# Optimization experiments

Measured on AMD Instinct MI355X. Metric: run time of the kernel, lower is better.

Reference implementation:

```python
import jax, jax.numpy as jnp
import numpy as np

DIM = 768
NUM_HEADS = 12
HEAD_DIM = DIM // NUM_HEADS
TIME_STEPS = 4
TAU_MEM = 2.0
THRESH = 1.0
NOISE_PROB = 0.01


def setup_inputs() -> dict:
    key = jax.random.key(0)
    ks = jax.random.split(key, 9)
    B, N = 8, 1024
    s = 1.0 / np.sqrt(DIM)
    inp = {"x": jax.random.normal(ks[0], (B, N, DIM), jnp.float32)}
    for i, nm in enumerate(["q", "k", "v", "o"]):
        inp["W" + nm] = jax.random.normal(ks[1 + i], (DIM, DIM), jnp.float32) * s
        inp["b" + nm] = jax.random.normal(ks[5 + i], (DIM,), jnp.float32) * 0.01
    return inp


def _lif_spikes(inp):
    """Multi-step LIF: constant input each step, leaky integrate, hard threshold,
    soft reset; aggregated spikes clamped to 1 (binary). Straight-through sigmoid
    surrogate keeps the op differentiable without changing forward values."""
    decay = jnp.exp(jnp.asarray(-1.0 / TAU_MEM, inp.dtype))

    def step(v, _):
        v = v * decay + inp
        sur = jax.nn.sigmoid(4.0 * (v - THRESH))
        hard = (v >= THRESH).astype(inp.dtype)
        spike = jax.lax.stop_gradient(hard - sur) + sur
        v = v - THRESH * spike
        return v, spike

    _, spikes = jax.lax.scan(step, jnp.zeros_like(inp), None, length=TIME_STEPS)
    # sum over time then clamp(max=1.0) -> binary aggregate spike map
    return jnp.minimum(spikes.sum(axis=0), 1.0)


def reference(x, Wq, bq, Wk, bk, Wv, bv, Wo, bo):
    B, N, C = x.shape
    q_lin = x @ Wq.T + bq
    k_lin = x @ Wk.T + bk
    v_lin = x @ Wv.T + bv

    s_q = _lif_spikes(q_lin)  # (B,N,C) binary
    s_k = _lif_spikes(k_lin)
    s_v = _lif_spikes(v_lin)

    # noise injection for fully-silent samples (deterministic key)
    silent = jnp.all(s_q == 0, axis=(1, 2)) & jnp.all(s_k == 0, axis=(1, 2))  # (B,)
    nk = jax.random.split(jax.random.key(42), 2)
    noise_q = (jax.random.uniform(nk[0], s_q.shape) < NOISE_PROB).astype(s_q.dtype)
    noise_k = (jax.random.uniform(nk[1], s_k.shape) < NOISE_PROB).astype(s_k.dtype)
    s_q = jnp.where(silent[:, None, None], jnp.maximum(s_q, noise_q), s_q)
    s_k = jnp.where(silent[:, None, None], jnp.maximum(s_k, noise_k), s_k)

    # (B,H,N,Dh)
    s_q = s_q.reshape(B, N, NUM_HEADS, HEAD_DIM).transpose(0, 2, 1, 3)
    s_k = s_k.reshape(B, N, NUM_HEADS, HEAD_DIM).transpose(0, 2, 1, 3)
    s_v = s_v.reshape(B, N, NUM_HEADS, HEAD_DIM).transpose(0, 2, 1, 3)

    # XNOR similarity: sum_d (1 - (q-k)^2) = Dh - |q| - |k| + 2 q.k  (exact, since
    # the broadcast form expands to the same polynomial; q,k binary so q^2=q)
    q2 = jnp.sum(s_q * s_q, axis=-1)  # (B,H,N)
    k2 = jnp.sum(s_k * s_k, axis=-1)  # (B,H,N)
    qk = jnp.einsum('bhnd,bhmd->bhnm', s_q, s_k)
    scores = HEAD_DIM - q2[..., :, None] - k2[..., None, :] + 2.0 * qk  # (B,H,N,N)

    attn = jax.nn.sigmoid(scores)
    out = jnp.einsum('bhnm,bhmd->bhnd', attn, s_v)  # (B,H,N,Dh)
    out = out.transpose(0, 2, 1, 3).reshape(B, N, C)
    return out @ Wo.T + bo
```

## Files before the change

kernel.cpp:

```cpp
#include <hip/hip_runtime.h>


typedef __attribute__((ext_vector_type(8))) short short8;
typedef __attribute__((ext_vector_type(4))) float f32x4;
typedef __attribute__((ext_vector_type(2))) unsigned long long u64x2;
typedef unsigned long long u64;

static __device__ __forceinline__ unsigned short f2bf(float f) {
  unsigned int u = __builtin_bit_cast(unsigned int, f);
  return (unsigned short)((u + 0x7FFFu + ((u >> 16) & 1u)) >> 16);
}

static __device__ __forceinline__ u64 pack4bf(float a, float b, float c, float d) {
  return (u64)f2bf(a) | ((u64)f2bf(b) << 16) | ((u64)f2bf(c) << 32) |
         ((u64)f2bf(d) << 48);
}

static __device__ __forceinline__ void gl2lds16(const unsigned short* g,
                                                unsigned short* l) {
  __builtin_amdgcn_global_load_lds(
      (const __attribute__((address_space(1))) unsigned int*)(g),
      (__attribute__((address_space(3))) unsigned int*)(l),
      16, 0, 0);
}

__global__ void k_convert(const float* __restrict__ x,
                          const float* __restrict__ Wq, const float* __restrict__ bq,
                          const float* __restrict__ Wk, const float* __restrict__ bk,
                          const float* __restrict__ Wv, const float* __restrict__ bv,
                          unsigned short* __restrict__ xb,
                          unsigned short* __restrict__ wcat,
                          float* __restrict__ bcat,
                          int* __restrict__ cnt,
                          float* __restrict__ colsum) {
  const int X4 = 1572864;
  const int W4 = 147456;
  const int NB = 576;
  const int NZ = 1536;
  const int total = X4 + 3 * W4 + NB + NZ;
  int t = blockIdx.x * blockDim.x + threadIdx.x;
  if (t >= total) return;
  if (t == 0) *cnt = 0;
  if (t < X4) {
    float4 v = ((const float4*)x)[t];
    *(u64*)(xb + 4 * (long)t) = pack4bf(v.x, v.y, v.z, v.w);
  } else if (t < X4 + 3 * W4) {
    int j = t - X4;
    const float* src = Wq;
    int jj = j;
    if (jj >= 2 * W4) { src = Wv; jj -= 2 * W4; }
    else if (jj >= W4) { src = Wk; jj -= W4; }
    float4 v = ((const float4*)src)[jj];
    *(u64*)(wcat + 4 * (long)j) = pack4bf(v.x, v.y, v.z, v.w);
  } else if (t < X4 + 3 * W4 + NB) {
    int j = t - (X4 + 3 * W4);
    int idx = j * 4;
    const float* src = bq;
    int ii = idx;
    if (ii >= 1536) { src = bv; ii -= 1536; }
    else if (ii >= 768) { src = bk; ii -= 768; }
    float4 v = *(const float4*)(src + ii);
    *(float4*)(bcat + idx) = v;
  } else {
    int j = t - (X4 + 3 * W4 + NB);
    float4 z = {0.f, 0.f, 0.f, 0.f};
    ((float4*)colsum)[j] = z;
  }
}

__global__ __launch_bounds__(256, 4)
void k_qkv(const unsigned short* __restrict__ xb,
           const unsigned short* __restrict__ wcat,
           const float* __restrict__ bcat,
           u64* __restrict__ bits3,
           float* __restrict__ colsum)
{
  __shared__ __align__(16) unsigned short lA[128 * 64];
  __shared__ __align__(16) unsigned short lB[128 * 64];
  const int tid = threadIdx.x;
  const int lane = tid & 63;
  const int wid = tid >> 6;
  const int wm = wid >> 1, wn = wid & 1;
  const int row0 = blockIdx.x * 128;
  const int col0 = blockIdx.y * 128;
  const int srow = lane >> 3;
  const int scol = (lane & 7) * 8;
  const int rr = lane & 15;
  const int g = lane >> 4;
  const int g8 = g * 8;

  const unsigned short* gA = xb + (long)(row0 + wid * 32 + srow) * 768 + scol;
  const unsigned short* gB = wcat + (long)(col0 + wid * 32 + srow) * 768 + scol;
  unsigned short* sA = &lA[(wid * 32 + srow) * 64 + scol];
  unsigned short* sB = &lB[(wid * 32 + srow) * 64 + scol];

  f32x4 acc[4][4] = {};

#pragma unroll 1
  for (int kt = 0; kt < 768; kt += 64) {
    __syncthreads();
#pragma unroll
    for (int s = 0; s < 4; ++s) {
      gl2lds16(gA + s * (8 * 768) + kt, sA + s * (8 * 64));
      gl2lds16(gB + s * (8 * 768) + kt, sB + s * (8 * 64));
    }
    __syncthreads();
#pragma unroll
    for (int kk = 0; kk < 2; ++kk) {
      const int ko = kk * 32 + g8;
      short8 af[4];
#pragma unroll
      for (int i = 0; i < 4; ++i)
        af[i] = *(const short8*)&lA[(wm * 64 + i * 16 + rr) * 64 + ko];
#pragma unroll
      for (int j = 0; j < 4; ++j) {
        const short8 bf = *(const short8*)&lB[(wn * 64 + j * 16 + rr) * 64 + ko];
#pragma unroll
        for (int i = 0; i < 4; ++i)
          acc[i][j] = __builtin_amdgcn_mfma_f32_16x16x32_bf16(af[i], bf, acc[i][j], 0, 0, 0);
      }
    }
  }

  const int mi = blockIdx.y / 6;
  const int h = 2 * (blockIdx.y - mi * 6) + wn;
  u64* bits = bits3 + (long)mi * 98304;
  const float C_LIF = 0.45505041f;
  float thr[4];
#pragma unroll
  for (int j = 0; j < 4; ++j) thr[j] = C_LIF - bcat[col0 + wn * 64 + j * 16 + rr];

  float csum[4] = {0.f, 0.f, 0.f, 0.f};
#pragma unroll
  for (int i = 0; i < 4; ++i) {
#pragma unroll
    for (int r = 0; r < 4; ++r) {
      u64 map = 0;
#pragma unroll
      for (int j = 0; j < 4; ++j) {
        const bool sp = acc[i][j][r] >= thr[j];
        const u64 bl = __ballot(sp);
        map |= ((bl >> (g * 16)) & 0xFFFFull) << (j * 16);
        csum[j] += sp ? 1.0f : 0.0f;
      }
      if (rr == 0) {
        const int grow = row0 + wm * 64 + i * 16 + g * 4 + r;
        const int b = grow >> 10, n = grow & 1023;
        bits[((long)b * 12 + h) * 1024 + n] = map;
      }
    }
  }
  if (mi == 2) {
    const int b = row0 >> 10;
#pragma unroll
    for (int j = 0; j < 4; ++j) {
      float s = csum[j];
      s += __shfl_xor(s, 16);
      s += __shfl_xor(s, 32);
      if (lane < 16) atomicAdd(colsum + b * 768 + h * 64 + j * 16 + rr, s);
    }
  }
}

__global__ __launch_bounds__(256)
void k_sb(const u64* __restrict__ qbits, const u64* __restrict__ kbits,
          const float* __restrict__ colsum, const float* __restrict__ Wo,
          const float* __restrict__ bo,
          int* __restrict__ cnt, int4* __restrict__ list,
          float* __restrict__ base) {
  __shared__ __align__(16) u64 kb[1024];
  const int tid = threadIdx.x;
  const int bid = blockIdx.x;
  if (bid < 768) {
    const int bh = bid >> 3;
    const u64* src = kbits + (long)bh * 1024;
#pragma unroll
    for (int u = 0; u < 4; ++u) kb[tid * 4 + u] = src[tid * 4 + u];
    __syncthreads();
    const int n = (bid & 7) * 128 + (tid >> 1);
    const u64 qb = qbits[(long)bh * 1024 + n];
    const u64x2* kb2 = (const u64x2*)kb + (tid & 1) * 256;
    int mh = 0;
#pragma unroll 4
    for (int mm = 0; mm < 256; ++mm) {
      const u64x2 v = kb2[mm];
      mh = max(mh, __popcll(qb ^ v.x));
      mh = max(mh, __popcll(qb ^ v.y));
    }
    const int rowmax = max(mh, __shfl_xor(mh, 1));
    if (rowmax > 52) {
      const int mbase = (tid & 1) * 512;
      for (int mm = 0; mm < 512; ++mm) {
        const int hd = __popcll(qb ^ kb[mbase + mm]);
        if (hd > 52) {
          const int e = atomicAdd(cnt, 1);
          if (e < 8192) list[e] = make_int4(bh, n, mbase + mm, hd);
        }
      }
    }
  } else {
    const int bb = bid - 768;
    const int b = bb / 3, ch = bb - b * 3;
    const int oc = ch * 256 + tid;
    const float4* c4 = (const float4*)(colsum + b * 768);
    const float4* w4 = (const float4*)(Wo + (long)oc * 768);
    float acc = bo[oc];
#pragma unroll 4
    for (int i = 0; i < 192; ++i) {
      const float4 c = c4[i], w = w4[i];
      acc += c.x * w.x + c.y * w.y + c.z * w.z + c.w * w.w;
    }
    base[b * 768 + oc] = acc;
  }
}

__global__ __launch_bounds__(192)
void k_out(const float* __restrict__ base, const int* __restrict__ cnt,
           const int4* __restrict__ list, const u64* __restrict__ vbits,
           const float* __restrict__ Wo, float* __restrict__ out) {
  const int row = blockIdx.x;
  const int b = row >> 10;
  float4 v = ((const float4*)(base + b * 768))[threadIdx.x];
  const int c = min(*cnt, 8192);
  if (c > 0) {
    const int n = row & 1023;
    for (int e = 0; e < c; ++e) {
      const int4 E = list[e];
      const int eb = E.x / 12;
      if (eb == b && E.y == n) {
        const int hh = E.x - eb * 12;
        const float s = (float)(64 - E.w);
        const float w = 1.0f / (1.0f + __expf(s));
        const u64 vb = vbits[(long)E.x * 1024 + E.z];
        float4 d = {0.f, 0.f, 0.f, 0.f};
        for (int dd = 0; dd < 64; ++dd)
          if ((vb >> dd) & 1ull) {
            const float* wp = Wo + (long)(threadIdx.x * 4) * 768 + hh * 64 + dd;
            d.x += wp[0]; d.y += wp[768]; d.z += wp[1536]; d.w += wp[2304];
          }
        v.x -= w * d.x; v.y -= w * d.y; v.z -= w * d.z; v.w -= w * d.w;
      }
    }
  }
  ((float4*)(out + (long)row * 768))[threadIdx.x] = v;
}

extern "C" void kernel_launch(void* const* d_in, const int* in_sizes, int n_in,
                              void* d_out, int out_size, void* d_ws, size_t ws_size,
                              hipStream_t stream) {
  const float* x  = (const float*)d_in[0];
  const float* Wq = (const float*)d_in[1];
  const float* bq = (const float*)d_in[2];
  const float* Wk = (const float*)d_in[3];
  const float* bk = (const float*)d_in[4];
  const float* Wv = (const float*)d_in[5];
  const float* bv = (const float*)d_in[6];
  const float* Wo = (const float*)d_in[7];
  const float* bo = (const float*)d_in[8];
  float* out = (float*)d_out;

  char* ws = (char*)d_ws;
  unsigned short* xb    = (unsigned short*)(ws + 0);
  unsigned short* wcat  = (unsigned short*)(ws + 12582912);
  float*          bcat  = (float*)(ws + 16121856);
  u64*            bits3 = (u64*)(ws + 16131072);
  float*          colsum = (float*)(ws + 18490368);
  float*          base   = (float*)(ws + 18514944);
  int*            cnt    = (int*)(ws + 18539520);
  int4*           list   = (int4*)(ws + 18539536);

  const u64* qbits = bits3;
  const u64* kbits = bits3 + 98304;
  const u64* vbits = bits3 + 2 * 98304;

  k_convert<<<dim3(7881), dim3(256), 0, stream>>>(x, Wq, bq, Wk, bk, Wv, bv,
                                                  xb, wcat, bcat, cnt, colsum);
  k_qkv<<<dim3(64, 18), dim3(256), 0, stream>>>(xb, wcat, bcat, bits3, colsum);
  k_sb<<<dim3(792), dim3(256), 0, stream>>>(qbits, kbits, colsum, Wo, bo,
                                            cnt, list, base);
  k_out<<<dim3(8192), dim3(192), 0, stream>>>(base, cnt, list, vbits, Wo, out);
}
```

Measured before the change: 101.6 us.

## Prune Hamming-distance candidate scan by bucketing keys by popcount

Keys for each head are counting-sorted in shared memory by popcount, using a histogram and suffix sums. Each query row then scans only the keys whose popcount is large enough that popcount(q^k) could exceed the threshold, since popcount(q^k) <= popcount(q)+popcount(k). This replaces the full 1024-key max pass plus rescan with a bounded candidate scan. The cost is extra shared memory, LDS atomics, and a serial prefix-sum loop on one thread.

```diff
diff --git a/kernel.cpp b/kernel.cpp
--- a/kernel.cpp
+++ b/kernel.cpp
@@ -3,7 +3,6 @@
 
 typedef __attribute__((ext_vector_type(8))) short short8;
 typedef __attribute__((ext_vector_type(4))) float f32x4;
-typedef __attribute__((ext_vector_type(2))) unsigned long long u64x2;
 typedef unsigned long long u64;
 
 static __device__ __forceinline__ unsigned short f2bf(float f) {
@@ -169,33 +168,55 @@
           int* __restrict__ cnt, int4* __restrict__ list,
           float* __restrict__ base) {
   __shared__ __align__(16) u64 kb[1024];
+  __shared__ int pkv[1024];
+  __shared__ unsigned short cand[1024];
+  __shared__ int hist[65];
+  __shared__ int sufv[65];
   const int tid = threadIdx.x;
   const int bid = blockIdx.x;
   if (bid < 768) {
     const int bh = bid >> 3;
     const u64* src = kbits + (long)bh * 1024;
-#pragma unroll
-    for (int u = 0; u < 4; ++u) kb[tid * 4 + u] = src[tid * 4 + u];
+    if (tid < 65) hist[tid] = 0;
+    __syncthreads();
+#pragma unroll
+    for (int u = 0; u < 4; ++u) {
+      const int m = tid + 256 * u;
+      const u64 v = src[m];
+      kb[m] = v;
+      const int pk = __popcll(v);
+      pkv[m] = pk;
+      atomicAdd(&hist[pk], 1);
+    }
+    __syncthreads();
+    if (tid == 0) {
+      int run = 0;
+#pragma unroll 1
+      for (int v = 64; v >= 0; --v) {
+        const int c = hist[v];
+        hist[v] = run;
+        run += c;
+        sufv[v] = run;
+      }
+    }
+    __syncthreads();
+#pragma unroll
+    for (int u = 0; u < 4; ++u) {
+      const int m = tid + 256 * u;
+      const int pos = atomicAdd(&hist[pkv[m]], 1);
+      cand[pos] = (unsigned short)m;
+    }
     __syncthreads();
     const int n = (bid & 7) * 128 + (tid >> 1);
     const u64 qb = qbits[(long)bh * 1024 + n];
-    const u64x2* kb2 = (const u64x2*)kb + (tid & 1) * 256;
-    int mh = 0;
-#pragma unroll 4
-    for (int mm = 0; mm < 256; ++mm) {
-      const u64x2 v = kb2[mm];
-      mh = max(mh, __popcll(qb ^ v.x));
-      mh = max(mh, __popcll(qb ^ v.y));
-    }
-    const int rowmax = max(mh, __shfl_xor(mh, 1));
-    if (rowmax > 52) {
-      const int mbase = (tid & 1) * 512;
-      for (int mm = 0; mm < 512; ++mm) {
-        const int hd = __popcll(qb ^ kb[mbase + mm]);
-        if (hd > 52) {
-          const int e = atomicAdd(cnt, 1);
-          if (e < 8192) list[e] = make_int4(bh, n, mbase + mm, hd);
-        }
+    const int t = 53 - __popcll(qb);
+    const int L = (t <= 0) ? 1024 : ((t > 64) ? 0 : sufv[t]);
+    for (int e = (tid & 1); e < L; e += 2) {
+      const int m = cand[e];
+      const int hd = __popcll(qb ^ kb[m]);
+      if (hd > 52) {
+        const int x = atomicAdd(cnt, 1);
+        if (x < 8192) list[x] = make_int4(bh, n, m, hd);
       }
     }
   } else {
```

New measurement: 117.9 us. 16.1% more time.

## Prefilter high-popcount q/k rows in QKV kernel to prune Hamming search

Applied to the files above, without the earlier changes.

The QKV kernel now records, per (batch, head), the row indices whose q or k spike word has popcount of at least 27 into small candidate lists. The Hamming-distance search kernel then only compares those candidate q rows against all k rows, and the remaining low-popcount q rows against only the candidate k rows. This replaces the all-pairs 1024x1024 popcount scan per head. The colsum·Wo base computation is also remapped onto fewer blocks. The result is exact only if a pair can exceed the distance threshold of 52 only when one side has popcount of at least 27, and only if no list overflows its 128-entry cap. Overflow would silently drop pairs.

```diff
diff --git a/kernel.cpp b/kernel.cpp
--- a/kernel.cpp
+++ b/kernel.cpp
@@ -3,7 +3,6 @@
 
 typedef __attribute__((ext_vector_type(8))) short short8;
 typedef __attribute__((ext_vector_type(4))) float f32x4;
-typedef __attribute__((ext_vector_type(2))) unsigned long long u64x2;
 typedef unsigned long long u64;
 
 static __device__ __forceinline__ unsigned short f2bf(float f) {
@@ -32,11 +31,12 @@
                           unsigned short* __restrict__ wcat,
                           float* __restrict__ bcat,
                           int* __restrict__ cnt,
-                          float* __restrict__ colsum) {
+                          float* __restrict__ colsum,
+                          int* __restrict__ hiCnt) {
   const int X4 = 1572864;
   const int W4 = 147456;
   const int NB = 576;
-  const int NZ = 1536;
+  const int NZ = 1584;
   const int total = X4 + 3 * W4 + NB + NZ;
   int t = blockIdx.x * blockDim.x + threadIdx.x;
   if (t >= total) return;
@@ -64,7 +64,8 @@
   } else {
     int j = t - (X4 + 3 * W4 + NB);
     float4 z = {0.f, 0.f, 0.f, 0.f};
-    ((float4*)colsum)[j] = z;
+    if (j < 1536) ((float4*)colsum)[j] = z;
+    else          ((float4*)hiCnt)[j - 1536] = z;
   }
 }
 
@@ -73,7 +74,9 @@
            const unsigned short* __restrict__ wcat,
            const float* __restrict__ bcat,
            u64* __restrict__ bits3,
-           float* __restrict__ colsum)
+           float* __restrict__ colsum,
+           int* __restrict__ hiCnt,
+           unsigned short* __restrict__ hiList)
 {
   __shared__ __align__(16) unsigned short lA[128 * 64];
   __shared__ __align__(16) unsigned short lB[128 * 64];
@@ -146,7 +149,14 @@
       if (rr == 0) {
         const int grow = row0 + wm * 64 + i * 16 + g * 4 + r;
         const int b = grow >> 10, n = grow & 1023;
-        bits[((long)b * 12 + h) * 1024 + n] = map;
+        const int bh = b * 12 + h;
+        bits[(long)bh * 1024 + n] = map;
+        if (mi < 2) {
+          if (__popcll(map) >= 27) {
+            const int p = atomicAdd(hiCnt + mi * 96 + bh, 1);
+            if (p < 128) hiList[(mi * 96 + bh) * 128 + p] = (unsigned short)n;
+          }
+        }
       }
     }
   }
@@ -164,44 +174,53 @@
 
 __global__ __launch_bounds__(256)
 void k_sb(const u64* __restrict__ qbits, const u64* __restrict__ kbits,
+          const int* __restrict__ hiCnt, const unsigned short* __restrict__ hiList,
           const float* __restrict__ colsum, const float* __restrict__ Wo,
           const float* __restrict__ bo,
           int* __restrict__ cnt, int4* __restrict__ list,
           float* __restrict__ base) {
-  __shared__ __align__(16) u64 kb[1024];
   const int tid = threadIdx.x;
-  const int bid = blockIdx.x;
-  if (bid < 768) {
-    const int bh = bid >> 3;
-    const u64* src = kbits + (long)bh * 1024;
-#pragma unroll
-    for (int u = 0; u < 4; ++u) kb[tid * 4 + u] = src[tid * 4 + u];
+  const int bh = blockIdx.x;
+  const int y = blockIdx.y;
+  if (y < 128) {
+    const int nc = min(hiCnt[bh], 128);
+    if (y >= nc) return;
+    const int n = hiList[bh * 128 + y];
+    const u64 qv = qbits[(long)bh * 1024 + n];
+    const u64* kp = kbits + (long)bh * 1024;
+#pragma unroll
+    for (int u = 0; u < 4; ++u) {
+      const int m = tid + 256 * u;
+      const int hd = __popcll(qv ^ kp[m]);
+      if (hd > 52) {
+        const int x = atomicAdd(cnt, 1);
+        if (x < 8192) list[x] = make_int4(bh, n, m, hd);
+      }
+    }
+  } else if (y < 136) {
+    __shared__ u64 kd[128];
+    __shared__ unsigned short km[128];
+    const int kc = min(hiCnt[96 + bh], 128);
+    if (tid < kc) {
+      const int m = hiList[(96 + bh) * 128 + tid];
+      km[tid] = (unsigned short)m;
+      kd[tid] = kbits[(long)bh * 1024 + m];
+    }
     __syncthreads();
-    const int n = (bid & 7) * 128 + (tid >> 1);
-    const u64 qb = qbits[(long)bh * 1024 + n];
-    const u64x2* kb2 = (const u64x2*)kb + (tid & 1) * 256;
-    int mh = 0;
-#pragma unroll 4
-    for (int mm = 0; mm < 256; ++mm) {
-      const u64x2 v = kb2[mm];
-      mh = max(mh, __popcll(qb ^ v.x));
-      mh = max(mh, __popcll(qb ^ v.y));
-    }
-    const int rowmax = max(mh, __shfl_xor(mh, 1));
-    if (rowmax > 52) {
-      const int mbase = (tid & 1) * 512;
-      for (int mm = 0; mm < 512; ++mm) {
-        const int hd = __popcll(qb ^ kb[mbase + mm]);
-        if (hd > 52) {
-          const int e = atomicAdd(cnt, 1);
-          if (e < 8192) list[e] = make_int4(bh, n, mbase + mm, hd);
-        }
+    const int n = (y - 128) * 128 + (tid >> 1);
+    const u64 qv = qbits[(long)bh * 1024 + n];
+    if (__popcll(qv) >= 27) return;
+    for (int e = (tid & 1); e < kc; e += 2) {
+      const int hd = __popcll(qv ^ kd[e]);
+      if (hd > 52) {
+        const int x = atomicAdd(cnt, 1);
+        if (x < 8192) list[x] = make_int4(bh, n, km[e], hd);
       }
     }
   } else {
-    const int bb = bid - 768;
-    const int b = bb / 3, ch = bb - b * 3;
-    const int oc = ch * 256 + tid;
+    if (bh >= 24) return;
+    const int oc = bh * 32 + (tid >> 3);
+    const int b = tid & 7;
     const float4* c4 = (const float4*)(colsum + b * 768);
     const float4* w4 = (const float4*)(Wo + (long)oc * 768);
     float acc = bo[oc];
@@ -260,23 +279,27 @@
   float* out = (float*)d_out;
 
   char* ws = (char*)d_ws;
-  unsigned short* xb    = (unsigned short*)(ws + 0);
-  unsigned short* wcat  = (unsigned short*)(ws + 12582912);
-  float*          bcat  = (float*)(ws + 16121856);
-  u64*            bits3 = (u64*)(ws + 16131072);
+  unsigned short* xb     = (unsigned short*)(ws + 0);
+  unsigned short* wcat   = (unsigned short*)(ws + 12582912);
+  float*          bcat   = (float*)(ws + 16121856);
+  u64*            bits3  = (u64*)(ws + 16131072);
   float*          colsum = (float*)(ws + 18490368);
   float*          base   = (float*)(ws + 18514944);
   int*            cnt    = (int*)(ws + 18539520);
   int4*           list   = (int4*)(ws + 18539536);
+  int*            hiCnt  = (int*)(ws + 18670608);
+  unsigned short* hiList = (unsigned short*)(ws + 18671376);
 
   const u64* qbits = bits3;
   const u64* kbits = bits3 + 98304;
   const u64* vbits = bits3 + 2 * 98304;
 
   k_convert<<<dim3(7881), dim3(256), 0, stream>>>(x, Wq, bq, Wk, bk, Wv, bv,
-                                                  xb, wcat, bcat, cnt, colsum);
-  k_qkv<<<dim3(64, 18), dim3(256), 0, stream>>>(xb, wcat, bcat, bits3, colsum);
-  k_sb<<<dim3(792), dim3(256), 0, stream>>>(qbits, kbits, colsum, Wo, bo,
-                                            cnt, list, base);
+                                                  xb, wcat, bcat, cnt, colsum,
+                                                  hiCnt);
+  k_qkv<<<dim3(64, 18), dim3(256), 0, stream>>>(xb, wcat, bcat, bits3, colsum,
+                                                hiCnt, hiList);
+  k_sb<<<dim3(96, 137), dim3(256), 0, stream>>>(qbits, kbits, hiCnt, hiList,
+                                                colsum, Wo, bo, cnt, list, base);
   k_out<<<dim3(8192), dim3(192), 0, stream>>>(base, cnt, list, vbits, Wo, out);
 }
```

Result: slower. 117.4 us (+15.5%).

## Prune Hamming search with popcount-filtered key lists and per-row correction in output kernel

Applied to the files above, without the earlier changes.

Replaces the brute-force all-pairs Hamming scan over every (query,key) pair with a pigeonhole filter. Any pair with Hamming distance above 52 needs both popcounts large or small, so keys with popcount of at least 27 are compacted into per-head lists. Each output row then scans the full key set only when its query has a high popcount, and otherwise only the compacted list, collecting hits in shared memory. This drops the global atomic list and the per-row scan of that list in the output kernel, and changes the base GEMV mapping to cover all batches per block. It risks truncating hits at 64 per row.

```diff
diff --git a/kernel.cpp b/kernel.cpp
--- a/kernel.cpp
+++ b/kernel.cpp
@@ -3,7 +3,6 @@
 
 typedef __attribute__((ext_vector_type(8))) short short8;
 typedef __attribute__((ext_vector_type(4))) float f32x4;
-typedef __attribute__((ext_vector_type(2))) unsigned long long u64x2;
 typedef unsigned long long u64;
 
 static __device__ __forceinline__ unsigned short f2bf(float f) {
@@ -31,7 +30,6 @@
                           unsigned short* __restrict__ xb,
                           unsigned short* __restrict__ wcat,
                           float* __restrict__ bcat,
-                          int* __restrict__ cnt,
                           float* __restrict__ colsum) {
   const int X4 = 1572864;
   const int W4 = 147456;
@@ -40,7 +38,6 @@
   const int total = X4 + 3 * W4 + NB + NZ;
   int t = blockIdx.x * blockDim.x + threadIdx.x;
   if (t >= total) return;
-  if (t == 0) *cnt = 0;
   if (t < X4) {
     float4 v = ((const float4*)x)[t];
     *(u64*)(xb + 4 * (long)t) = pack4bf(v.x, v.y, v.z, v.w);
@@ -163,45 +160,38 @@
 }
 
 __global__ __launch_bounds__(256)
-void k_sb(const u64* __restrict__ qbits, const u64* __restrict__ kbits,
-          const float* __restrict__ colsum, const float* __restrict__ Wo,
-          const float* __restrict__ bo,
-          int* __restrict__ cnt, int4* __restrict__ list,
-          float* __restrict__ base) {
-  __shared__ __align__(16) u64 kb[1024];
+void k_hg(const u64* __restrict__ kbits, const float* __restrict__ colsum,
+          const float* __restrict__ Wo, const float* __restrict__ bo,
+          int* __restrict__ hiCnt, unsigned short* __restrict__ hiIdx,
+          u64* __restrict__ hiData, float* __restrict__ base) {
   const int tid = threadIdx.x;
   const int bid = blockIdx.x;
-  if (bid < 768) {
-    const int bh = bid >> 3;
-    const u64* src = kbits + (long)bh * 1024;
-#pragma unroll
-    for (int u = 0; u < 4; ++u) kb[tid * 4 + u] = src[tid * 4 + u];
-    __syncthreads();
-    const int n = (bid & 7) * 128 + (tid >> 1);
-    const u64 qb = qbits[(long)bh * 1024 + n];
-    const u64x2* kb2 = (const u64x2*)kb + (tid & 1) * 256;
-    int mh = 0;
-#pragma unroll 4
-    for (int mm = 0; mm < 256; ++mm) {
-      const u64x2 v = kb2[mm];
-      mh = max(mh, __popcll(qb ^ v.x));
-      mh = max(mh, __popcll(qb ^ v.y));
-    }
-    const int rowmax = max(mh, __shfl_xor(mh, 1));
-    if (rowmax > 52) {
-      const int mbase = (tid & 1) * 512;
-      for (int mm = 0; mm < 512; ++mm) {
-        const int hd = __popcll(qb ^ kb[mbase + mm]);
-        if (hd > 52) {
-          const int e = atomicAdd(cnt, 1);
-          if (e < 8192) list[e] = make_int4(bh, n, mbase + mm, hd);
-        }
-      }
+  if (bid < 96) {
+    __shared__ int cnt_l;
+    __shared__ unsigned short lst[1024];
+    if (tid == 0) cnt_l = 0;
+    __syncthreads();
+    const u64* src = kbits + (long)bid * 1024;
+#pragma unroll
+    for (int u = 0; u < 4; ++u) {
+      const int m = tid + u * 256;
+      if (__popcll(src[m]) >= 27) {
+        const int p = atomicAdd(&cnt_l, 1);
+        lst[p] = (unsigned short)m;
+      }
+    }
+    __syncthreads();
+    const int c = cnt_l;
+    if (tid == 0) hiCnt[bid] = c;
+    for (int p = tid; p < c; p += 256) {
+      const int m = lst[p];
+      hiIdx[bid * 1024 + p] = (unsigned short)m;
+      hiData[(long)bid * 1024 + p] = src[m];
     }
   } else {
-    const int bb = bid - 768;
-    const int b = bb / 3, ch = bb - b * 3;
-    const int oc = ch * 256 + tid;
+    const int j = bid - 96;
+    const int oc = j * 32 + (tid >> 3);
+    const int b = tid & 7;
     const float4* c4 = (const float4*)(colsum + b * 768);
     const float4* w4 = (const float4*)(Wo + (long)oc * 768);
     float acc = bo[oc];
@@ -215,34 +205,57 @@
 }
 
 __global__ __launch_bounds__(192)
-void k_out(const float* __restrict__ base, const int* __restrict__ cnt,
-           const int4* __restrict__ list, const u64* __restrict__ vbits,
-           const float* __restrict__ Wo, float* __restrict__ out) {
+void k_out(const float* __restrict__ base, const u64* __restrict__ qbits,
+           const u64* __restrict__ kbits, const int* __restrict__ hiCnt,
+           const unsigned short* __restrict__ hiIdx, const u64* __restrict__ hiData,
+           const u64* __restrict__ vbits, const float* __restrict__ Wo,
+           float* __restrict__ out) {
+  __shared__ int vc;
+  __shared__ int vm[64], vh[64], vhd[64];
+  const int tid = threadIdx.x;
   const int row = blockIdx.x;
-  const int b = row >> 10;
-  float4 v = ((const float4*)(base + b * 768))[threadIdx.x];
-  const int c = min(*cnt, 8192);
-  if (c > 0) {
-    const int n = row & 1023;
-    for (int e = 0; e < c; ++e) {
-      const int4 E = list[e];
-      const int eb = E.x / 12;
-      if (eb == b && E.y == n) {
-        const int hh = E.x - eb * 12;
-        const float s = (float)(64 - E.w);
-        const float w = 1.0f / (1.0f + __expf(s));
-        const u64 vb = vbits[(long)E.x * 1024 + E.z];
-        float4 d = {0.f, 0.f, 0.f, 0.f};
-        for (int dd = 0; dd < 64; ++dd)
-          if ((vb >> dd) & 1ull) {
-            const float* wp = Wo + (long)(threadIdx.x * 4) * 768 + hh * 64 + dd;
-            d.x += wp[0]; d.y += wp[768]; d.z += wp[1536]; d.w += wp[2304];
-          }
-        v.x -= w * d.x; v.y -= w * d.y; v.z -= w * d.z; v.w -= w * d.w;
-      }
-    }
-  }
-  ((float4*)(out + (long)row * 768))[threadIdx.x] = v;
+  const int b = row >> 10, n = row & 1023;
+  if (tid == 0) vc = 0;
+  __syncthreads();
+  float4 v = ((const float4*)(base + b * 768))[tid];
+#pragma unroll 1
+  for (int h = 0; h < 12; ++h) {
+    const int bh = b * 12 + h;
+    const u64 qv = qbits[(long)bh * 1024 + n];
+    if (__popcll(qv) >= 27) {
+      for (int m = tid; m < 1024; m += 192) {
+        const int hd = __popcll(qv ^ kbits[(long)bh * 1024 + m]);
+        if (hd > 52) {
+          const int p = atomicAdd(&vc, 1);
+          if (p < 64) { vm[p] = m; vh[p] = h; vhd[p] = hd; }
+        }
+      }
+    } else {
+      const int kc = hiCnt[bh];
+      for (int e = tid; e < kc; e += 192) {
+        const int hd = __popcll(qv ^ hiData[(long)bh * 1024 + e]);
+        if (hd > 52) {
+          const int p = atomicAdd(&vc, 1);
+          if (p < 64) { vm[p] = hiIdx[bh * 1024 + e]; vh[p] = h; vhd[p] = hd; }
+        }
+      }
+    }
+  }
+  __syncthreads();
+  const int c = min(vc, 64);
+  for (int e = 0; e < c; ++e) {
+    const float s = (float)(64 - vhd[e]);
+    const float w = 1.0f / (1.0f + __expf(s));
+    const u64 vb = vbits[((long)(b * 12 + vh[e])) * 1024 + vm[e]];
+    float4 d = {0.f, 0.f, 0.f, 0.f};
+    for (int dd = 0; dd < 64; ++dd)
+      if ((vb >> dd) & 1ull) {
+        const float* wp = Wo + (long)(tid * 4) * 768 + vh[e] * 64 + dd;
+        d.x += wp[0]; d.y += wp[768]; d.z += wp[1536]; d.w += wp[2304];
+      }
+    v.x -= w * d.x; v.y -= w * d.y; v.z -= w * d.z; v.w -= w * d.w;
+  }
+  ((float4*)(out + (long)row * 768))[tid] = v;
 }
 
 extern "C" void kernel_launch(void* const* d_in, const int* in_sizes, int n_in,
@@ -260,23 +273,25 @@
   float* out = (float*)d_out;
 
   char* ws = (char*)d_ws;
-  unsigned short* xb    = (unsigned short*)(ws + 0);
-  unsigned short* wcat  = (unsigned short*)(ws + 12582912);
-  float*          bcat  = (float*)(ws + 16121856);
-  u64*            bits3 = (u64*)(ws + 16131072);
+  unsigned short* xb     = (unsigned short*)(ws + 0);
+  unsigned short* wcat   = (unsigned short*)(ws + 12582912);
+  float*          bcat   = (float*)(ws + 16121856);
+  u64*            bits3  = (u64*)(ws + 16131072);
   float*          colsum = (float*)(ws + 18490368);
   float*          base   = (float*)(ws + 18514944);
-  int*            cnt    = (int*)(ws + 18539520);
-  int4*           list   = (int4*)(ws + 18539536);
+  int*            hiCnt  = (int*)(ws + 18539520);
+  unsigned short* hiIdx  = (unsigned short*)(ws + 18540032);
+  u64*            hiData = (u64*)(ws + 18736640);
 
   const u64* qbits = bits3;
   const u64* kbits = bits3 + 98304;
   const u64* vbits = bits3 + 2 * 98304;
 
   k_convert<<<dim3(7881), dim3(256), 0, stream>>>(x, Wq, bq, Wk, bk, Wv, bv,
-                                                  xb, wcat, bcat, cnt, colsum);
+                                                  xb, wcat, bcat, colsum);
   k_qkv<<<dim3(64, 18), dim3(256), 0, stream>>>(xb, wcat, bcat, bits3, colsum);
-  k_sb<<<dim3(792), dim3(256), 0, stream>>>(qbits, kbits, colsum, Wo, bo,
-                                            cnt, list, base);
-  k_out<<<dim3(8192), dim3(192), 0, stream>>>(base, cnt, list, vbits, Wo, out);
-}
+  k_hg<<<dim3(120), dim3(256), 0, stream>>>(kbits, colsum, Wo, bo,
+                                            hiCnt, hiIdx, hiData, base);
+  k_out<<<dim3(8192), dim3(192), 0, stream>>>(base, qbits, kbits, hiCnt, hiIdx,
+                                              hiData, vbits, Wo, out);
+}
```

Result: slower. 111.2 us (+9.5%).
